# Performance work log

Hardware: AMD Instinct MI355X
Metric: run time of the kernel (lower is better)

The kernel has to match this reference:

```python
import jax, jax.numpy as jnp
from jax import lax
import numpy as np

B, S, V, H, C = 128, 512, 128, 1024, 10
E = H // 4  # embed_dim = hidden_dim / 4 per the module


def setup_inputs() -> dict:
    key = jax.random.key(0)
    ks = jax.random.split(key, 16)

    def kaiming(k, shape):
        fan_in = shape[0]
        return jax.random.normal(k, shape, dtype=jnp.float32) * np.sqrt(2.0 / fan_in)

    return {
        "x": jax.random.randint(ks[0], (B, 1, S), 0, V),
        "embedding": jax.random.normal(ks[1], (V, E), dtype=jnp.float32),
        "W_gx": kaiming(ks[2], (E, H)), "W_gh": kaiming(ks[3], (H, H)), "b_g": jnp.zeros((H,), jnp.float32),
        "W_ix": kaiming(ks[4], (E, H)), "W_ih": kaiming(ks[5], (H, H)), "b_i": jnp.zeros((H,), jnp.float32),
        "W_fx": kaiming(ks[6], (E, H)), "W_fh": kaiming(ks[7], (H, H)), "b_f": jnp.zeros((H,), jnp.float32),
        "W_ox": kaiming(ks[8], (E, H)), "W_oh": kaiming(ks[9], (H, H)), "b_o": jnp.zeros((H,), jnp.float32),
        "W_ph": kaiming(ks[10], (H, C)), "b_p": jnp.zeros((C,), jnp.float32),
    }


def reference(x, embedding, W_gx, W_gh, b_g, W_ix, W_ih, b_i,
              W_fx, W_fh, b_f, W_ox, W_oh, b_o, W_ph, b_p):
    batch = x.shape[0]
    hid = W_gh.shape[0]
    # embed whole sequence at once: [B, S, E]
    xe = embedding[x[:, 0, :]]
    # fuse the 4 input-side GEMMs into one: [B, S, 4H] (precomputable, parallel over time)
    Wx = jnp.concatenate([W_gx, W_ix, W_fx, W_ox], axis=1)  # [E, 4H]
    Wh = jnp.concatenate([W_gh, W_ih, W_fh, W_oh], axis=1)  # [H, 4H]
    b = jnp.concatenate([b_g, b_i, b_f, b_o])               # [4H]
    xproj = jnp.einsum('bse,ef->sbf', xe, Wx) + b           # [S, B, 4H] (time-major for scan)

    def step(carry, xp_t):
        h, c = carry
        z = xp_t + h @ Wh  # [B, 4H]
        g = jnp.tanh(z[:, :hid])
        i = jax.nn.sigmoid(z[:, hid:2 * hid])
        f = jax.nn.sigmoid(z[:, 2 * hid:3 * hid])
        o = jax.nn.sigmoid(z[:, 3 * hid:])
        c = g * i + c * f
        h = jnp.tanh(c) * o
        return (h, c), None

    h0 = jnp.zeros((batch, hid), xproj.dtype)
    c0 = jnp.zeros((batch, hid), xproj.dtype)
    (h, _), _ = lax.scan(step, (h0, c0), xproj)

    p = h @ W_ph + b_p
    return jax.nn.log_softmax(p, axis=1)
```

## Files before the change

kernel.cpp:

```cpp
#include <hip/hip_runtime.h>

#define H_ 1024
#define B_ 128
#define S_ 512
#define V_ 128
#define E_ 256

#define ZSH_OFF 0
#define TSH_OFF 67584
#define HSH_OFF 135168
#define XSH_OFF 136192
#define SMEM_TOTAL 136256

#define HXBUF 131072

typedef __bf16 bf16x8 __attribute__((ext_vector_type(8)));
typedef float f32x4 __attribute__((ext_vector_type(4)));
typedef unsigned long long ull;

__device__ __forceinline__ uint4 cload16(const unsigned short* p) {
  uint4 r;
  asm volatile("global_load_dwordx4 %0, %1, off sc0 sc1"
               : "=v"(r) : "v"(p) : "memory");
  return r;
}
__device__ __forceinline__ void cstore8(unsigned short* p, ull v) {
  __hip_atomic_store((ull*)p, v, __ATOMIC_RELAXED, __HIP_MEMORY_SCOPE_AGENT);
}

__device__ __forceinline__ unsigned short f2bf(float f) {
  unsigned u = __float_as_uint(f);
  u += 0x7fffu + ((u >> 16) & 1u);
  return (unsigned short)(u >> 16);
}
__device__ __forceinline__ float sigf(float x) { return 1.0f / (1.0f + __expf(-x)); }
__device__ __forceinline__ float tanhfast(float x) { return 1.0f - 2.0f / (1.0f + __expf(2.0f * x)); }

__global__ void __launch_bounds__(256)
tokproj_kernel(const float* __restrict__ emb,
               const float* __restrict__ Wgx, const float* __restrict__ Wix,
               const float* __restrict__ Wfx, const float* __restrict__ Wox,
               const float* __restrict__ bg, const float* __restrict__ bi,
               const float* __restrict__ bf_, const float* __restrict__ bo,
               float* __restrict__ tokproj) {
  __shared__ float esh[E_];
  const int v = blockIdx.x;
  const int c = blockIdx.y * 256 + threadIdx.x;
  const int gate = c >> 10;
  const int j = c & 1023;
  const float* W = (gate == 0) ? Wgx : (gate == 1) ? Wix : (gate == 2) ? Wfx : Wox;
  const float* bias = (gate == 0) ? bg : (gate == 1) ? bi : (gate == 2) ? bf_ : bo;
  esh[threadIdx.x] = emb[v * E_ + threadIdx.x];
  __syncthreads();
  float acc = bias[j];
#pragma unroll 4
  for (int e = 0; e < E_; ++e) acc += esh[e] * W[e * H_ + j];
  tokproj[v * 4096 + c] = acc;
}

__global__ void __launch_bounds__(256)
wht_kernel(const float* __restrict__ Wgh, const float* __restrict__ Wih,
           const float* __restrict__ Wfh, const float* __restrict__ Woh,
           unsigned short* __restrict__ WhT) {
  const int c = blockIdx.x;
  const int gate = c >> 10;
  const int j = c & 1023;
  const float* W = (gate == 0) ? Wgh : (gate == 1) ? Wih : (gate == 2) ? Wfh : Woh;
  for (int k = threadIdx.x; k < H_; k += 256)
    WhT[c * H_ + k] = f2bf(W[k * H_ + j]);
}

__global__ void __launch_bounds__(256)
xpose_kernel(const int* __restrict__ x, int* __restrict__ xT) {
  const int id = blockIdx.x * 256 + threadIdx.x;
  const int s = id >> 7, b = id & 127;
  xT[s * 128 + b] = x[b * S_ + s];
}

__global__ void __launch_bounds__(512, 1)
lstm_scan(const int* __restrict__ xT, const float* __restrict__ tokproj,
          const unsigned short* __restrict__ WhT,
          unsigned short* __restrict__ hX, float* __restrict__ hfin,
          unsigned* __restrict__ pub) {
  extern __shared__ char smem[];
  float* Zsh = (float*)(smem + ZSH_OFF);
  float* tsh = (float*)(smem + TSH_OFF);
  unsigned short* hsh = (unsigned short*)(smem + HSH_OFF);
  int* xsh = (int*)(smem + XSH_OFF);

  const int bid = blockIdx.x;
  const int rg = bid >> 5;
  const int cg = bid & 31;
  const int tid = threadIdx.x;
  const int w = tid >> 6;
  const int lane = tid & 63;
  const int l15 = lane & 15;
  const int lq = lane >> 4;

  for (int it = tid; it < 16384; it += 512) {
    const int v = it >> 7, j = it & 127;
    tsh[v * 132 + j] = tokproj[v * 4096 + (j >> 5) * 1024 + cg * 32 + (j & 31)];
  }
  uint4 breg[32];
#pragma unroll
  for (int kc = 0; kc < 4; ++kc) {
#pragma unroll
    for (int t = 0; t < 8; ++t) {
      const int j = t * 16 + l15;
      const int c = ((j >> 5) << 10) + cg * 32 + (j & 31);
      breg[kc * 8 + t] =
          *(const uint4*)(WhT + c * 1024 + (w * 4 + kc) * 32 + lq * 8);
    }
  }

  const int row_own = tid >> 5;
  const int hu = tid & 31;
  const int brow = rg * 16 + row_own;
  const int colg = cg * 32 + hu;

  const unsigned* myflag = pub + (rg * 32 + w * 4 + (lane & 3)) * 32;
  const unsigned short* abase[4];
#pragma unroll
  for (int kc = 0; kc < 4; ++kc)
    abase[kc] = hX + (rg * 32 + w * 4 + kc) * 512 + lane * 8;

  float creg = 0.f;
  if (tid < 128) cstore8(hX + bid * 512 + tid * 4, 0ull);
  asm volatile("s_waitcnt vmcnt(0)" ::: "memory");
  __syncthreads();
  if (tid == 0)
    __hip_atomic_store(pub + bid * 32, 1u, __ATOMIC_RELAXED, __HIP_MEMORY_SCOPE_AGENT);

  for (int s = 0; s < S_; ++s) {
    int xv = 0;
    if (tid < 16) xv = xT[s * 128 + rg * 16 + tid];

    const unsigned tgt = (unsigned)(s + 1);
    while (__hip_atomic_load(myflag, __ATOMIC_RELAXED, __HIP_MEMORY_SCOPE_AGENT) < tgt)
      __builtin_amdgcn_s_sleep(1);

    const int soff = (s & 1) * HXBUF;
    uint4 a[4];
#pragma unroll
    for (int kc = 0; kc < 4; ++kc) a[kc] = cload16(abase[kc] + soff);
    asm volatile("s_waitcnt vmcnt(0)" ::: "memory");
    __builtin_amdgcn_sched_barrier(0);
#pragma unroll
    for (int kc = 0; kc < 4; ++kc) {
      asm volatile("" : "+v"(a[kc].x), "+v"(a[kc].y), "+v"(a[kc].z), "+v"(a[kc].w));
    }

    if (tid < 16) xsh[tid] = xv;

    f32x4 acc[8];
#pragma unroll
    for (int t = 0; t < 8; ++t) acc[t] = (f32x4){0.f, 0.f, 0.f, 0.f};
#pragma unroll
    for (int kc = 0; kc < 4; ++kc) {
      const bf16x8 av = __builtin_bit_cast(bf16x8, a[kc]);
#pragma unroll
      for (int t = 0; t < 8; ++t)
        acc[t] = __builtin_amdgcn_mfma_f32_16x16x32_bf16(
            av, __builtin_bit_cast(bf16x8, breg[kc * 8 + t]), acc[t], 0, 0, 0);
    }
#pragma unroll
    for (int t = 0; t < 8; ++t) {
#pragma unroll
      for (int r_ = 0; r_ < 4; ++r_)
        Zsh[(w * 16 + lq * 4 + r_) * 132 + t * 16 + l15] = acc[t][r_];
    }
    __syncthreads();

    {
      const int xb = xsh[row_own];
      const float* tp = tsh + xb * 132;
      float z[4];
#pragma unroll
      for (int gate = 0; gate < 4; ++gate) {
        float zz = tp[gate * 32 + hu];
#pragma unroll
        for (int w8 = 0; w8 < 8; ++w8)
          zz += Zsh[(w8 * 16 + row_own) * 132 + gate * 32 + hu];
        z[gate] = zz;
      }
      const float gv = tanhfast(z[0]);
      const float iv = sigf(z[1]);
      const float fv = sigf(z[2]);
      const float ov = sigf(z[3]);
      creg = gv * iv + creg * fv;
      const float hv = tanhfast(creg) * ov;
      hsh[row_own * 32 + hu] = f2bf(hv);
      if (s == S_ - 1) hfin[brow * H_ + colg] = hv;
    }
    __syncthreads();

    if (tid < 64) {
      const ull* hp = (const ull*)hsh;
      const int si = (tid & 15) * 8 + (tid >> 4) * 2;
      unsigned short* dst = hX + ((s + 1) & 1) * HXBUF + bid * 512 + tid * 8;
      cstore8(dst, hp[si]);
      cstore8(dst + 4, hp[si + 1]);
      asm volatile("s_waitcnt vmcnt(0)" ::: "memory");
      if (tid == 0)
        __hip_atomic_store(pub + bid * 32, (unsigned)(s + 2),
                           __ATOMIC_RELAXED, __HIP_MEMORY_SCOPE_AGENT);
    }
  }
}

__global__ void __launch_bounds__(256)
classify_kernel(const float* __restrict__ hfin, const float* __restrict__ Wph,
                const float* __restrict__ bp, float* __restrict__ out) {
  __shared__ float red[256 * 10];
  const int b = blockIdx.x, tid = threadIdx.x;
  float acc[10];
#pragma unroll
  for (int c = 0; c < 10; ++c) acc[c] = 0.f;
  for (int k = tid; k < H_; k += 256) {
    const float hv = hfin[b * H_ + k];
    const float* w = Wph + k * 10;
#pragma unroll
    for (int c = 0; c < 10; ++c) acc[c] += hv * w[c];
  }
#pragma unroll
  for (int c = 0; c < 10; ++c) red[tid * 10 + c] = acc[c];
  __syncthreads();
  for (int off = 128; off >= 1; off >>= 1) {
    if (tid < off) {
#pragma unroll
      for (int c = 0; c < 10; ++c) red[tid * 10 + c] += red[(tid + off) * 10 + c];
    }
    __syncthreads();
  }
  if (tid == 0) {
    float p[10];
    float m = -1e30f;
#pragma unroll
    for (int c = 0; c < 10; ++c) { p[c] = red[c] + bp[c]; m = fmaxf(m, p[c]); }
    float ssum = 0.f;
#pragma unroll
    for (int c = 0; c < 10; ++c) ssum += __expf(p[c] - m);
    const float lse = m + __logf(ssum);
#pragma unroll
    for (int c = 0; c < 10; ++c) out[b * 10 + c] = p[c] - lse;
  }
}

extern "C" void kernel_launch(void* const* d_in, const int* in_sizes, int n_in,
                              void* d_out, int out_size, void* d_ws, size_t ws_size,
                              hipStream_t stream) {
  (void)in_sizes; (void)n_in; (void)out_size; (void)ws_size;
  const int* x = (const int*)d_in[0];
  const float* emb = (const float*)d_in[1];
  const float* Wgx = (const float*)d_in[2];
  const float* Wgh = (const float*)d_in[3];
  const float* bg = (const float*)d_in[4];
  const float* Wix = (const float*)d_in[5];
  const float* Wih = (const float*)d_in[6];
  const float* bi = (const float*)d_in[7];
  const float* Wfx = (const float*)d_in[8];
  const float* Wfh = (const float*)d_in[9];
  const float* bf_ = (const float*)d_in[10];
  const float* Wox = (const float*)d_in[11];
  const float* Woh = (const float*)d_in[12];
  const float* bo = (const float*)d_in[13];
  const float* Wph = (const float*)d_in[14];
  const float* bp = (const float*)d_in[15];
  float* out = (float*)d_out;

  char* ws = (char*)d_ws;
  float* tokproj = (float*)ws;
  unsigned short* WhT = (unsigned short*)(ws + 2097152);
  unsigned short* hX = (unsigned short*)(ws + 10485760);
  float* hfin = (float*)(ws + 11010048);
  int* xT = (int*)(ws + 11538432);
  unsigned* pub = (unsigned*)(ws + 11800576);

  (void)hipMemsetAsync(pub, 0, 32768, stream);
  (void)hipFuncSetAttribute(reinterpret_cast<const void*>(lstm_scan),
                            hipFuncAttributeMaxDynamicSharedMemorySize, SMEM_TOTAL);

  tokproj_kernel<<<dim3(V_, 16), dim3(256), 0, stream>>>(
      emb, Wgx, Wix, Wfx, Wox, bg, bi, bf_, bo, tokproj);
  wht_kernel<<<dim3(4096), dim3(256), 0, stream>>>(Wgh, Wih, Wfh, Woh, WhT);
  xpose_kernel<<<dim3(256), dim3(256), 0, stream>>>(x, xT);
  lstm_scan<<<dim3(256), dim3(512), SMEM_TOTAL, stream>>>(
      xT, tokproj, WhT, hX, hfin, pub);
  classify_kernel<<<dim3(128), dim3(256), 0, stream>>>(hfin, Wph, bp, out);
}
```

Measured before the change: 1.741 ms.

## Fuse prep kernels and interleave gate values in shared memory for vector access

Merges the token-projection, recurrent-weight transpose and index transpose kernels into one launch, split by block index. It also changes the shared-memory layout of the partial gate sums and token projections so the four gates of a hidden unit sit next to each other, padded to a 33-unit stride. Each thread can then read and reduce them with 128-bit vector loads instead of 36 scalar loads. The aim is fewer LDS instructions per timestep on the serial critical path, at the cost of more scattered scalar-to-vector writes after the MFMA stage and possible bank conflicts from the new stride.

```diff
diff --git a/kernel.cpp b/kernel.cpp
--- a/kernel.cpp
+++ b/kernel.cpp
@@ -37,44 +37,43 @@
 __device__ __forceinline__ float tanhfast(float x) { return 1.0f - 2.0f / (1.0f + __expf(2.0f * x)); }
 
 __global__ void __launch_bounds__(256)
-tokproj_kernel(const float* __restrict__ emb,
-               const float* __restrict__ Wgx, const float* __restrict__ Wix,
-               const float* __restrict__ Wfx, const float* __restrict__ Wox,
-               const float* __restrict__ bg, const float* __restrict__ bi,
-               const float* __restrict__ bf_, const float* __restrict__ bo,
-               float* __restrict__ tokproj) {
+prep_kernel(const float* __restrict__ emb,
+            const float* __restrict__ Wgx, const float* __restrict__ Wix,
+            const float* __restrict__ Wfx, const float* __restrict__ Wox,
+            const float* __restrict__ bg, const float* __restrict__ bi,
+            const float* __restrict__ bf_, const float* __restrict__ bo,
+            const float* __restrict__ Wgh, const float* __restrict__ Wih,
+            const float* __restrict__ Wfh, const float* __restrict__ Woh,
+            const int* __restrict__ x,
+            float* __restrict__ tokproj, unsigned short* __restrict__ WhT,
+            int* __restrict__ xT) {
   __shared__ float esh[E_];
-  const int v = blockIdx.x;
-  const int c = blockIdx.y * 256 + threadIdx.x;
-  const int gate = c >> 10;
-  const int j = c & 1023;
-  const float* W = (gate == 0) ? Wgx : (gate == 1) ? Wix : (gate == 2) ? Wfx : Wox;
-  const float* bias = (gate == 0) ? bg : (gate == 1) ? bi : (gate == 2) ? bf_ : bo;
-  esh[threadIdx.x] = emb[v * E_ + threadIdx.x];
-  __syncthreads();
-  float acc = bias[j];
+  const int bid = blockIdx.x;
+  if (bid < 2048) {
+    const int v = bid >> 4;
+    const int c = (bid & 15) * 256 + threadIdx.x;
+    const int gate = c >> 10;
+    const int j = c & 1023;
+    const float* W = (gate == 0) ? Wgx : (gate == 1) ? Wix : (gate == 2) ? Wfx : Wox;
+    const float* bias = (gate == 0) ? bg : (gate == 1) ? bi : (gate == 2) ? bf_ : bo;
+    esh[threadIdx.x] = emb[v * E_ + threadIdx.x];
+    __syncthreads();
+    float acc = bias[j];
 #pragma unroll 4
-  for (int e = 0; e < E_; ++e) acc += esh[e] * W[e * H_ + j];
-  tokproj[v * 4096 + c] = acc;
-}
-
-__global__ void __launch_bounds__(256)
-wht_kernel(const float* __restrict__ Wgh, const float* __restrict__ Wih,
-           const float* __restrict__ Wfh, const float* __restrict__ Woh,
-           unsigned short* __restrict__ WhT) {
-  const int c = blockIdx.x;
-  const int gate = c >> 10;
-  const int j = c & 1023;
-  const float* W = (gate == 0) ? Wgh : (gate == 1) ? Wih : (gate == 2) ? Wfh : Woh;
-  for (int k = threadIdx.x; k < H_; k += 256)
-    WhT[c * H_ + k] = f2bf(W[k * H_ + j]);
-}
-
-__global__ void __launch_bounds__(256)
-xpose_kernel(const int* __restrict__ x, int* __restrict__ xT) {
-  const int id = blockIdx.x * 256 + threadIdx.x;
-  const int s = id >> 7, b = id & 127;
-  xT[s * 128 + b] = x[b * S_ + s];
+    for (int e = 0; e < E_; ++e) acc += esh[e] * W[e * H_ + j];
+    tokproj[v * 4096 + c] = acc;
+  } else if (bid < 6144) {
+    const int c = bid - 2048;
+    const int gate = c >> 10;
+    const int j = c & 1023;
+    const float* W = (gate == 0) ? Wgh : (gate == 1) ? Wih : (gate == 2) ? Wfh : Woh;
+    for (int k = threadIdx.x; k < H_; k += 256)
+      WhT[c * H_ + k] = f2bf(W[k * H_ + j]);
+  } else {
+    const int id = (bid - 6144) * 256 + threadIdx.x;
+    const int s = id >> 7, b = id & 127;
+    xT[s * 128 + b] = x[b * S_ + s];
+  }
 }
 
 __global__ void __launch_bounds__(512, 1)
@@ -99,7 +98,8 @@
 
   for (int it = tid; it < 16384; it += 512) {
     const int v = it >> 7, j = it & 127;
-    tsh[v * 132 + j] = tokproj[v * 4096 + (j >> 5) * 1024 + cg * 32 + (j & 31)];
+    const int gate = j >> 5, hu = j & 31;
+    tsh[(v * 33 + hu) * 4 + gate] = tokproj[v * 4096 + gate * 1024 + cg * 32 + hu];
   }
   uint4 breg[32];
 #pragma unroll
@@ -164,29 +164,25 @@
             av, __builtin_bit_cast(bf16x8, breg[kc * 8 + t]), acc[t], 0, 0, 0);
     }
 #pragma unroll
-    for (int t = 0; t < 8; ++t) {
-#pragma unroll
-      for (int r_ = 0; r_ < 4; ++r_)
-        Zsh[(w * 16 + lq * 4 + r_) * 132 + t * 16 + l15] = acc[t][r_];
+    for (int r_ = 0; r_ < 4; ++r_) {
+      const int row = w * 16 + lq * 4 + r_;
+      f32x4 lo = {acc[0][r_], acc[2][r_], acc[4][r_], acc[6][r_]};
+      f32x4 hi = {acc[1][r_], acc[3][r_], acc[5][r_], acc[7][r_]};
+      *(f32x4*)(Zsh + (row * 33 + l15) * 4) = lo;
+      *(f32x4*)(Zsh + (row * 33 + l15 + 16) * 4) = hi;
     }
     __syncthreads();
 
     {
       const int xb = xsh[row_own];
-      const float* tp = tsh + xb * 132;
-      float z[4];
-#pragma unroll
-      for (int gate = 0; gate < 4; ++gate) {
-        float zz = tp[gate * 32 + hu];
-#pragma unroll
-        for (int w8 = 0; w8 < 8; ++w8)
-          zz += Zsh[(w8 * 16 + row_own) * 132 + gate * 32 + hu];
-        z[gate] = zz;
-      }
-      const float gv = tanhfast(z[0]);
-      const float iv = sigf(z[1]);
-      const float fv = sigf(z[2]);
-      const float ov = sigf(z[3]);
+      f32x4 z4 = *(const f32x4*)(tsh + (xb * 33 + hu) * 4);
+#pragma unroll
+      for (int w8 = 0; w8 < 8; ++w8)
+        z4 += *(const f32x4*)(Zsh + ((w8 * 16 + row_own) * 33 + hu) * 4);
+      const float gv = tanhfast(z4[0]);
+      const float iv = sigf(z4[1]);
+      const float fv = sigf(z4[2]);
+      const float ov = sigf(z4[3]);
       creg = gv * iv + creg * fv;
       const float hv = tanhfast(creg) * ov;
       hsh[row_own * 32 + hu] = f2bf(hv);
@@ -280,10 +276,9 @@
   (void)hipFuncSetAttribute(reinterpret_cast<const void*>(lstm_scan),
                             hipFuncAttributeMaxDynamicSharedMemorySize, SMEM_TOTAL);
 
-  tokproj_kernel<<<dim3(V_, 16), dim3(256), 0, stream>>>(
-      emb, Wgx, Wix, Wfx, Wox, bg, bi, bf_, bo, tokproj);
-  wht_kernel<<<dim3(4096), dim3(256), 0, stream>>>(Wgh, Wih, Wfh, Woh, WhT);
-  xpose_kernel<<<dim3(256), dim3(256), 0, stream>>>(x, xT);
+  prep_kernel<<<dim3(6400), dim3(256), 0, stream>>>(
+      emb, Wgx, Wix, Wfx, Wox, bg, bi, bf_, bo,
+      Wgh, Wih, Wfh, Woh, x, tokproj, WhT, xT);
   lstm_scan<<<dim3(256), dim3(512), SMEM_TOTAL, stream>>>(
       xT, tokproj, WhT, hX, hfin, pub);
   classify_kernel<<<dim3(128), dim3(256), 0, stream>>>(hfin, Wph, bp, out);
```

Measured after the change: 1.709 ms. About the same (-1.8%).
